# Optimization experiments

Hardware: AMD Instinct MI355X
Metric: run time of the kernel (lower is better)

Reference implementation:

```python
import jax, jax.numpy as jnp
import numpy as np

EMBED_DIM = 128
NUM_HEADS = 4
HEAD_DIM = EMBED_DIM // NUM_HEADS


def setup_inputs() -> dict:
    key = jax.random.key(0)
    ks = jax.random.split(key, 12)
    B, N, D = 4, 4096, EMBED_DIM
    s = 1.0 / np.sqrt(D)
    inp = {
        "query": jax.random.normal(ks[0], (B, N, D), dtype=jnp.float32),
        "key": jax.random.normal(ks[1], (B, N, D), dtype=jnp.float32),
        "value": jax.random.normal(ks[2], (B, N, D), dtype=jnp.float32),
        "Wq": jax.random.uniform(ks[3], (D, D), jnp.float32, -s, s),
        "bq": jax.random.uniform(ks[4], (D,), jnp.float32, -s, s),
        "Wk": jax.random.uniform(ks[5], (D, D), jnp.float32, -s, s),
        "bk": jax.random.uniform(ks[6], (D,), jnp.float32, -s, s),
        "Wv": jax.random.uniform(ks[7], (D, D), jnp.float32, -s, s),
        "bv": jax.random.uniform(ks[8], (D,), jnp.float32, -s, s),
        "Wo": jax.random.uniform(ks[9], (D, D), jnp.float32, -s, s),
        "bo": jax.random.uniform(ks[10], (D,), jnp.float32, -s, s),
    }
    return inp


def reference(query, key, value, Wq, bq, Wk, bk, Wv, bv, Wo, bo):
    B, N, D = query.shape
    H, Dh = NUM_HEADS, HEAD_DIM
    scale = Dh ** -0.5
    # Linear projections (torch Linear: x @ W.T + b), split heads -> [B, H, N, Dh]
    Q = (query @ Wq.T + bq).reshape(B, N, H, Dh).transpose(0, 2, 1, 3)
    K = (key @ Wk.T + bk).reshape(B, N, H, Dh).transpose(0, 2, 1, 3)
    V = (value @ Wv.T + bv).reshape(B, N, H, Dh).transpose(0, 2, 1, 3)
    # Attention scores [B, H, N, N]
    scores = jnp.einsum('bhqd,bhkd->bhqk', Q, K) * scale
    attn = jax.nn.softmax(scores, axis=-1)
    ctx = jnp.einsum('bhqk,bhkd->bhqd', attn, V)  # [B, H, N, Dh]
    ctx = ctx.transpose(0, 2, 1, 3).reshape(B, N, D)
    return ctx @ Wo.T + bo
```

## Files before the change

kernel.cpp:

```cpp
#include <hip/hip_runtime.h>
#include <hip/hip_bf16.h>

#define N_SEQ 4096
#define DIM   128
#define NH    4
#define DH    32
#define BATCH 4

#define QSCALE 0.25503495870989204f

typedef __bf16 bf16x8 __attribute__((ext_vector_type(8)));
typedef __bf16 bf16x2 __attribute__((ext_vector_type(2)));
typedef __bf16 bf16x4 __attribute__((ext_vector_type(4)));
typedef float  f32x4  __attribute__((ext_vector_type(4)));

#define MFMA(a, b, c) __builtin_amdgcn_mfma_f32_16x16x32_bf16((a), (b), (c), 0, 0, 0)

static __device__ __forceinline__ bf16x8 cvt8(const float* __restrict__ p) {
    const float4* f4 = reinterpret_cast<const float4*>(p);
    float4 a = f4[0], b = f4[1];
    bf16x8 r;
    r[0] = (__bf16)a.x; r[1] = (__bf16)a.y; r[2] = (__bf16)a.z; r[3] = (__bf16)a.w;
    r[4] = (__bf16)b.x; r[5] = (__bf16)b.y; r[6] = (__bf16)b.z; r[7] = (__bf16)b.w;
    return r;
}

static __device__ __forceinline__ f32x4 exp4(f32x4 s) {
    f32x4 r;
    r[0] = __builtin_amdgcn_exp2f(s[0]);
    r[1] = __builtin_amdgcn_exp2f(s[1]);
    r[2] = __builtin_amdgcn_exp2f(s[2]);
    r[3] = __builtin_amdgcn_exp2f(s[3]);
    return r;
}

static __device__ __forceinline__ bf16x8 pack8(f32x4 a, f32x4 b) {
    bf16x8 o;
    o[0] = (__bf16)a[0]; o[1] = (__bf16)a[1];
    o[2] = (__bf16)a[2]; o[3] = (__bf16)a[3];
    o[4] = (__bf16)b[0]; o[5] = (__bf16)b[1];
    o[6] = (__bf16)b[2]; o[7] = (__bf16)b[3];
    return o;
}

__global__ __launch_bounds__(256) void proj_qkv(
    const float* __restrict__ xq, const float* __restrict__ xk, const float* __restrict__ xv,
    const float* __restrict__ Wq, const float* __restrict__ Wk, const float* __restrict__ Wv,
    const float* __restrict__ bq, const float* __restrict__ bk, const float* __restrict__ bv,
    __bf16* __restrict__ Qs, __bf16* __restrict__ Kb, __bf16* __restrict__ Vt)
{
    __shared__ __align__(16) char wlds[34816];
    const int z = blockIdx.z;
    const float* x    = (z == 0) ? xq : ((z == 1) ? xk : xv);
    const float* Wf   = (z == 0) ? Wq : ((z == 1) ? Wk : Wv);
    const float* bias = (z == 0) ? bq : ((z == 1) ? bk : bv);
    const int b    = blockIdx.y;
    const int tid  = threadIdx.x;
    const int wave = tid >> 6, lane = tid & 63;
    const int quad = lane >> 4, l15 = lane & 15;
    const int n0   = blockIdx.x * 64 + wave * 16;

    {
        const int r = tid >> 1, half = tid & 1;
        const float* wsrc = Wf + r * DIM + half * 64;
        char* wdst = wlds + r * 272 + half * 128;
        #pragma unroll
        for (int i = 0; i < 8; i++)
            *(bf16x8*)(wdst + i * 16) = cvt8(wsrc + i * 8);
    }

    bf16x8 a[4];
    const float* xrow = x + (b * N_SEQ + n0 + l15) * DIM + quad * 8;
    a[0] = cvt8(xrow);      a[1] = cvt8(xrow + 32);
    a[2] = cvt8(xrow + 64); a[3] = cvt8(xrow + 96);
    __syncthreads();

    const int n = n0 + l15;
    for (int t = 0; t < 8; t++) {
        const char* wr = wlds + (t * 16 + l15) * 272 + quad * 16;
        bf16x8 w0 = *(const bf16x8*)(wr);
        bf16x8 w1 = *(const bf16x8*)(wr + 64);
        bf16x8 w2 = *(const bf16x8*)(wr + 128);
        bf16x8 w3 = *(const bf16x8*)(wr + 192);

        f32x4 acc = {0.f, 0.f, 0.f, 0.f};
        acc = MFMA(w0, a[0], acc);
        acc = MFMA(w1, a[1], acc);
        acc = MFMA(w2, a[2], acc);
        acc = MFMA(w3, a[3], acc);

        const int d0 = t * 16 + quad * 4;
        if (z == 0) {
            const int h = d0 >> 5, dh0 = d0 & 31;
            bf16x4 q4;
            #pragma unroll
            for (int r = 0; r < 4; r++)
                q4[r] = (__bf16)((acc[r] + bias[d0 + r]) * QSCALE);
            *(bf16x4*)(Qs + ((b * NH + h) * N_SEQ + n) * DH + dh0) = q4;
        } else if (z == 1) {
            const int h = d0 >> 5, dh0 = d0 & 31;
            bf16x4 k4;
            #pragma unroll
            for (int r = 0; r < 4; r++)
                k4[r] = (__bf16)(acc[r] + bias[d0 + r]);
            *(bf16x4*)(Kb + ((b * NH + h) * N_SEQ + n) * DH + dh0) = k4;
        } else {
            const int nl = n & 63;
            const int np = (n & ~63) | (nl & 35) | ((nl & 12) << 1) | ((nl & 16) >> 2);
            #pragma unroll
            for (int r = 0; r < 4; r++) {
                const int d = d0 + r, h = d >> 5, dh = d & 31;
                Vt[((b * NH + h) * DH + dh) * N_SEQ + np] = (__bf16)(acc[r] + bias[d]);
            }
        }
    }
}

__global__ __launch_bounds__(256, 2) void flash_attn(
    const __bf16* __restrict__ Qs, const __bf16* __restrict__ Kb,
    const __bf16* __restrict__ Vt, __bf16* __restrict__ ctxb)
{
    __shared__ __align__(16) char smem[77824];
    char* const Kbase = smem;
    char* const Vbase = smem + 40960;

    const int bid  = blockIdx.x;
    const int bh   = bid & 15;
    const int qc   = bid >> 4;
    const int tid  = threadIdx.x;
    const int wave = tid >> 6, lane = tid & 63;
    const int quad = lane >> 4, l15 = lane & 15;
    const int qh   = wave & 1, kh = wave >> 1;
    const int n0   = qc * 128 + qh * 64;
    const int KH   = 2048;

    const __bf16* Qp = Qs + (bh * N_SEQ + n0) * DH;
    bf16x8 qf[4];
    #pragma unroll
    for (int q = 0; q < 4; q++)
        qf[q] = *(const bf16x8*)(Qp + (q * 16 + l15) * DH + quad * 8);

    const int r_ = tid >> 2, c_ = tid & 3;
    const __bf16* gK = Kb + (size_t)bh * N_SEQ * DH + r_ * DH + c_ * 8;
    const __bf16* gV = Vt + ((size_t)bh * DH + (tid >> 3)) * N_SEQ + (tid & 7) * 8;
    const int kofsK = r_ * 80 + c_ * 16;
    const int kofsV = (tid >> 3) * 144 + (tid & 7) * 16;

    {
        #pragma unroll
        for (int g = 0; g < 2; g++) {
            #pragma unroll
            for (int t = 0; t < 2; t++) {
                bf16x8 kr = *(const bf16x8*)(gK + (size_t)(g * KH + t * 64) * DH);
                bf16x8 vr = *(const bf16x8*)(gV + g * KH + t * 64);
                *(bf16x8*)(Kbase + g * 20480 + t * 5120 + kofsK) = kr;
                *(bf16x8*)(Vbase + g * 18432 + t * 4608 + kofsV) = vr;
            }
        }
    }
    __syncthreads();

    char* const Kme = Kbase + kh * 20480;
    char* const Vme = Vbase + kh * 18432;

    f32x4 c[4][2];
    #pragma unroll
    for (int q = 0; q < 4; q++) { c[q][0] = f32x4{0.f,0.f,0.f,0.f}; c[q][1] = f32x4{0.f,0.f,0.f,0.f}; }
    float l[4] = {0.f, 0.f, 0.f, 0.f};
    const f32x4 z4 = {0.f,0.f,0.f,0.f};

    for (int kbb = 0; kbb < KH / 128; kbb++) {
        const int cur = kbb & 1;
        const char* Kc = Kme + cur * 10240;
        const char* Vc = Vme + cur * 9216;

        const int kn = (kbb + 1) & (KH / 128 - 1);
        bf16x8 krn[2][2], vrn[2][2];
        #pragma unroll
        for (int g = 0; g < 2; g++) {
            #pragma unroll
            for (int t = 0; t < 2; t++) {
                krn[g][t] = *(const bf16x8*)(gK + (size_t)(g * KH + kn * 128 + t * 64) * DH);
                vrn[g][t] = *(const bf16x8*)(gV + g * KH + kn * 128 + t * 64);
            }
        }

        #pragma unroll
        for (int t = 0; t < 2; t++) {
            const char* Kt  = Kc + t * 5120;
            const char* Vtl = Vc + t * 4608;

            bf16x8 kf0 = *(const bf16x8*)(Kt + l15 * 80 + quad * 16);
            bf16x8 kf1 = *(const bf16x8*)(Kt + (16 + l15) * 80 + quad * 16);
            bf16x8 kf2 = *(const bf16x8*)(Kt + (32 + l15) * 80 + quad * 16);
            bf16x8 kf3 = *(const bf16x8*)(Kt + (48 + l15) * 80 + quad * 16);

            bf16x8 pf[4][2];
            #pragma unroll
            for (int q = 0; q < 4; q++) {
                f32x4 sa = MFMA(kf0, qf[q], z4);
                f32x4 sb = MFMA(kf1, qf[q], z4);
                f32x4 sc = MFMA(kf2, qf[q], z4);
                f32x4 sd = MFMA(kf3, qf[q], z4);
                f32x4 ea = exp4(sa), eb = exp4(sb), ec = exp4(sc), ed = exp4(sd);
                l[q] += ((ea[0]+ea[1])+(ea[2]+ea[3])) + ((eb[0]+eb[1])+(eb[2]+eb[3]))
                      + ((ec[0]+ec[1])+(ec[2]+ec[3])) + ((ed[0]+ed[1])+(ed[2]+ed[3]));
                pf[q][0] = pack8(ea, eb);
                pf[q][1] = pack8(ec, ed);
            }

            bf16x8 vf00 = *(const bf16x8*)(Vtl + l15 * 144 + quad * 16);
            bf16x8 vf10 = *(const bf16x8*)(Vtl + (16 + l15) * 144 + quad * 16);
            bf16x8 vf01 = *(const bf16x8*)(Vtl + l15 * 144 + 64 + quad * 16);
            bf16x8 vf11 = *(const bf16x8*)(Vtl + (16 + l15) * 144 + 64 + quad * 16);

            #pragma unroll
            for (int q = 0; q < 4; q++) {
                c[q][0] = MFMA(vf00, pf[q][0], c[q][0]);
                c[q][1] = MFMA(vf10, pf[q][0], c[q][1]);
                c[q][0] = MFMA(vf01, pf[q][1], c[q][0]);
                c[q][1] = MFMA(vf11, pf[q][1], c[q][1]);
            }
        }

        #pragma unroll
        for (int g = 0; g < 2; g++) {
            #pragma unroll
            for (int t = 0; t < 2; t++) {
                *(bf16x8*)(Kbase + g * 20480 + (cur ^ 1) * 10240 + t * 5120 + kofsK) = krn[g][t];
                *(bf16x8*)(Vbase + g * 18432 + (cur ^ 1) * 9216 + t * 4608 + kofsV) = vrn[g][t];
            }
        }
        __syncthreads();
    }

    #pragma unroll
    for (int q = 0; q < 4; q++) {
        l[q] += __shfl_xor(l[q], 16);
        l[q] += __shfl_xor(l[q], 32);
    }

    if (kh == 1) {
        char* dst = smem + (qh * 64 + lane) * 144;
        #pragma unroll
        for (int q = 0; q < 4; q++) {
            *(f32x4*)(dst + (q * 2 + 0) * 16) = c[q][0];
            *(f32x4*)(dst + (q * 2 + 1) * 16) = c[q][1];
        }
        f32x4 lv = {l[0], l[1], l[2], l[3]};
        *(f32x4*)(dst + 128) = lv;
    }
    __syncthreads();
    if (kh == 0) {
        const char* src = smem + (qh * 64 + lane) * 144;
        f32x4 lp = *(const f32x4*)(src + 128);
        const int b = bh >> 2, h = bh & 3;
        #pragma unroll
        for (int q = 0; q < 4; q++) {
            c[q][0] += *(const f32x4*)(src + (q * 2 + 0) * 16);
            c[q][1] += *(const f32x4*)(src + (q * 2 + 1) * 16);
            const float inv = 1.0f / (l[q] + lp[q]);
            const int qg = n0 + q * 16 + l15;
            __bf16* dst = ctxb + ((size_t)(b * N_SEQ + qg)) * DIM + h * DH + quad * 4;
            #pragma unroll
            for (int dt = 0; dt < 2; dt++) {
                f32x4 cc = c[q][dt];
                bf16x2 e0 = {(__bf16)(cc[0] * inv), (__bf16)(cc[1] * inv)};
                bf16x2 e1 = {(__bf16)(cc[2] * inv), (__bf16)(cc[3] * inv)};
                *(bf16x2*)(dst + dt * 16)     = e0;
                *(bf16x2*)(dst + dt * 16 + 2) = e1;
            }
        }
    }
}

__global__ __launch_bounds__(256) void out_proj(
    const __bf16* __restrict__ ctxb, const float* __restrict__ Wo,
    const float* __restrict__ bo, float* __restrict__ out)
{
    __shared__ __align__(16) char wlds[34816];
    const int b    = blockIdx.y;
    const int tid  = threadIdx.x;
    const int wave = tid >> 6, lane = tid & 63;
    const int quad = lane >> 4, l15 = lane & 15;
    const int n0   = blockIdx.x * 64 + wave * 16;

    {
        const int r = tid >> 1, half = tid & 1;
        const float* wsrc = Wo + r * DIM + half * 64;
        char* wdst = wlds + r * 272 + half * 128;
        #pragma unroll
        for (int i = 0; i < 8; i++)
            *(bf16x8*)(wdst + i * 16) = cvt8(wsrc + i * 8);
    }

    bf16x8 a[4];
    const __bf16* crow = ctxb + (b * N_SEQ + n0 + l15) * DIM + quad * 8;
    a[0] = *(const bf16x8*)(crow);
    a[1] = *(const bf16x8*)(crow + 32);
    a[2] = *(const bf16x8*)(crow + 64);
    a[3] = *(const bf16x8*)(crow + 96);
    __syncthreads();

    const int n = n0 + l15;
    for (int t = 0; t < 8; t++) {
        const char* wr = wlds + (t * 16 + l15) * 272 + quad * 16;
        bf16x8 w0 = *(const bf16x8*)(wr);
        bf16x8 w1 = *(const bf16x8*)(wr + 64);
        bf16x8 w2 = *(const bf16x8*)(wr + 128);
        bf16x8 w3 = *(const bf16x8*)(wr + 192);

        f32x4 acc = {0.f, 0.f, 0.f, 0.f};
        acc = MFMA(w0, a[0], acc);
        acc = MFMA(w1, a[1], acc);
        acc = MFMA(w2, a[2], acc);
        acc = MFMA(w3, a[3], acc);

        const int d0 = t * 16 + quad * 4;
        float4 o;
        o.x = acc[0] + bo[d0];
        o.y = acc[1] + bo[d0 + 1];
        o.z = acc[2] + bo[d0 + 2];
        o.w = acc[3] + bo[d0 + 3];
        *(float4*)(out + (b * N_SEQ + n) * DIM + d0) = o;
    }
}

extern "C" void kernel_launch(void* const* d_in, const int* in_sizes, int n_in,
                              void* d_out, int out_size, void* d_ws, size_t ws_size,
                              hipStream_t stream)
{
    const float* query = (const float*)d_in[0];
    const float* key   = (const float*)d_in[1];
    const float* value = (const float*)d_in[2];
    const float* Wq = (const float*)d_in[3];
    const float* bq = (const float*)d_in[4];
    const float* Wk = (const float*)d_in[5];
    const float* bk = (const float*)d_in[6];
    const float* Wv = (const float*)d_in[7];
    const float* bv = (const float*)d_in[8];
    const float* Wo = (const float*)d_in[9];
    const float* bo = (const float*)d_in[10];
    float* out = (float*)d_out;

    char* ws = (char*)d_ws;
    const size_t e = (size_t)BATCH * N_SEQ * DIM;
    __bf16* Qs   = (__bf16*)(ws);
    __bf16* Kb   = (__bf16*)(ws + 2 * e);
    __bf16* Vt   = (__bf16*)(ws + 4 * e);
    __bf16* ctxb = (__bf16*)(ws + 6 * e);

    proj_qkv<<<dim3(64, BATCH, 3), 256, 0, stream>>>(
        query, key, value, Wq, Wk, Wv, bq, bk, bv, Qs, Kb, Vt);
    flash_attn<<<dim3(512), 256, 0, stream>>>(Qs, Kb, Vt, ctxb);
    out_proj<<<dim3(64, BATCH), 256, 0, stream>>>(ctxb, Wo, bo, out);
}
```

Measured before the change: 149.7 us.

## Split flash attention keys four ways per block with 64-query blocks

Each block now covers 64 queries instead of 128, and its four waves each take one quarter of the key sequence instead of a 2x2 query/key split. The block count doubles and shared memory drops to about 38KB, so the launch bound is raised to allow four blocks per CU. The double-buffered LDS is replaced by a single buffer: fragments are read into registers, a barrier runs, then the next tile is written, which costs two barriers per step. Row sums are kept as vector accumulators, and the final reduction now merges three partial outputs through LDS instead of one.

```diff
diff --git a/kernel.cpp b/kernel.cpp
--- a/kernel.cpp
+++ b/kernel.cpp
@@ -116,23 +116,22 @@
     }
 }
 
-__global__ __launch_bounds__(256, 2) void flash_attn(
+__global__ __launch_bounds__(256, 4) void flash_attn(
     const __bf16* __restrict__ Qs, const __bf16* __restrict__ Kb,
     const __bf16* __restrict__ Vt, __bf16* __restrict__ ctxb)
 {
-    __shared__ __align__(16) char smem[77824];
+    __shared__ __align__(16) char smem[38912];
     char* const Kbase = smem;
-    char* const Vbase = smem + 40960;
+    char* const Vbase = smem + 20480;
 
     const int bid  = blockIdx.x;
     const int bh   = bid & 15;
     const int qc   = bid >> 4;
     const int tid  = threadIdx.x;
-    const int wave = tid >> 6, lane = tid & 63;
+    const int kh   = tid >> 6, lane = tid & 63;
     const int quad = lane >> 4, l15 = lane & 15;
-    const int qh   = wave & 1, kh = wave >> 1;
-    const int n0   = qc * 128 + qh * 64;
-    const int KH   = 2048;
+    const int n0   = qc * 64;
+    const int KH   = 1024;
 
     const __bf16* Qp = Qs + (bh * N_SEQ + n0) * DH;
     bf16x8 qf[4];
@@ -148,118 +147,111 @@
 
     {
         #pragma unroll
-        for (int g = 0; g < 2; g++) {
-            #pragma unroll
-            for (int t = 0; t < 2; t++) {
-                bf16x8 kr = *(const bf16x8*)(gK + (size_t)(g * KH + t * 64) * DH);
-                bf16x8 vr = *(const bf16x8*)(gV + g * KH + t * 64);
-                *(bf16x8*)(Kbase + g * 20480 + t * 5120 + kofsK) = kr;
-                *(bf16x8*)(Vbase + g * 18432 + t * 4608 + kofsV) = vr;
-            }
+        for (int g = 0; g < 4; g++) {
+            bf16x8 kr = *(const bf16x8*)(gK + (size_t)(g * KH) * DH);
+            bf16x8 vr = *(const bf16x8*)(gV + g * KH);
+            *(bf16x8*)(Kbase + g * 5120 + kofsK) = kr;
+            *(bf16x8*)(Vbase + g * 4608 + kofsV) = vr;
         }
     }
     __syncthreads();
 
-    char* const Kme = Kbase + kh * 20480;
-    char* const Vme = Vbase + kh * 18432;
+    char* const Kme = Kbase + kh * 5120;
+    char* const Vme = Vbase + kh * 4608;
 
     f32x4 c[4][2];
     #pragma unroll
     for (int q = 0; q < 4; q++) { c[q][0] = f32x4{0.f,0.f,0.f,0.f}; c[q][1] = f32x4{0.f,0.f,0.f,0.f}; }
-    float l[4] = {0.f, 0.f, 0.f, 0.f};
+    f32x4 lv[4];
+    #pragma unroll
+    for (int q = 0; q < 4; q++) lv[q] = f32x4{0.f,0.f,0.f,0.f};
     const f32x4 z4 = {0.f,0.f,0.f,0.f};
 
-    for (int kbb = 0; kbb < KH / 128; kbb++) {
-        const int cur = kbb & 1;
-        const char* Kc = Kme + cur * 10240;
-        const char* Vc = Vme + cur * 9216;
-
-        const int kn = (kbb + 1) & (KH / 128 - 1);
-        bf16x8 krn[2][2], vrn[2][2];
-        #pragma unroll
-        for (int g = 0; g < 2; g++) {
-            #pragma unroll
-            for (int t = 0; t < 2; t++) {
-                krn[g][t] = *(const bf16x8*)(gK + (size_t)(g * KH + kn * 128 + t * 64) * DH);
-                vrn[g][t] = *(const bf16x8*)(gV + g * KH + kn * 128 + t * 64);
-            }
-        }
-
-        #pragma unroll
-        for (int t = 0; t < 2; t++) {
-            const char* Kt  = Kc + t * 5120;
-            const char* Vtl = Vc + t * 4608;
-
-            bf16x8 kf0 = *(const bf16x8*)(Kt + l15 * 80 + quad * 16);
-            bf16x8 kf1 = *(const bf16x8*)(Kt + (16 + l15) * 80 + quad * 16);
-            bf16x8 kf2 = *(const bf16x8*)(Kt + (32 + l15) * 80 + quad * 16);
-            bf16x8 kf3 = *(const bf16x8*)(Kt + (48 + l15) * 80 + quad * 16);
-
-            bf16x8 pf[4][2];
-            #pragma unroll
-            for (int q = 0; q < 4; q++) {
-                f32x4 sa = MFMA(kf0, qf[q], z4);
-                f32x4 sb = MFMA(kf1, qf[q], z4);
-                f32x4 sc = MFMA(kf2, qf[q], z4);
-                f32x4 sd = MFMA(kf3, qf[q], z4);
-                f32x4 ea = exp4(sa), eb = exp4(sb), ec = exp4(sc), ed = exp4(sd);
-                l[q] += ((ea[0]+ea[1])+(ea[2]+ea[3])) + ((eb[0]+eb[1])+(eb[2]+eb[3]))
-                      + ((ec[0]+ec[1])+(ec[2]+ec[3])) + ((ed[0]+ed[1])+(ed[2]+ed[3]));
-                pf[q][0] = pack8(ea, eb);
-                pf[q][1] = pack8(ec, ed);
-            }
-
-            bf16x8 vf00 = *(const bf16x8*)(Vtl + l15 * 144 + quad * 16);
-            bf16x8 vf10 = *(const bf16x8*)(Vtl + (16 + l15) * 144 + quad * 16);
-            bf16x8 vf01 = *(const bf16x8*)(Vtl + l15 * 144 + 64 + quad * 16);
-            bf16x8 vf11 = *(const bf16x8*)(Vtl + (16 + l15) * 144 + 64 + quad * 16);
-
-            #pragma unroll
-            for (int q = 0; q < 4; q++) {
-                c[q][0] = MFMA(vf00, pf[q][0], c[q][0]);
-                c[q][1] = MFMA(vf10, pf[q][0], c[q][1]);
-                c[q][0] = MFMA(vf01, pf[q][1], c[q][0]);
-                c[q][1] = MFMA(vf11, pf[q][1], c[q][1]);
-            }
-        }
-
-        #pragma unroll
-        for (int g = 0; g < 2; g++) {
-            #pragma unroll
-            for (int t = 0; t < 2; t++) {
-                *(bf16x8*)(Kbase + g * 20480 + (cur ^ 1) * 10240 + t * 5120 + kofsK) = krn[g][t];
-                *(bf16x8*)(Vbase + g * 18432 + (cur ^ 1) * 9216 + t * 4608 + kofsV) = vrn[g][t];
-            }
-        }
+    for (int kb = 0; kb < KH / 64; kb++) {
+        const int kn = (kb + 1) & (KH / 64 - 1);
+        bf16x8 krn[4], vrn[4];
+        #pragma unroll
+        for (int g = 0; g < 4; g++) {
+            krn[g] = *(const bf16x8*)(gK + (size_t)(g * KH + kn * 64) * DH);
+            vrn[g] = *(const bf16x8*)(gV + g * KH + kn * 64);
+        }
+
+        bf16x8 kf0 = *(const bf16x8*)(Kme + l15 * 80 + quad * 16);
+        bf16x8 kf1 = *(const bf16x8*)(Kme + (16 + l15) * 80 + quad * 16);
+        bf16x8 kf2 = *(const bf16x8*)(Kme + (32 + l15) * 80 + quad * 16);
+        bf16x8 kf3 = *(const bf16x8*)(Kme + (48 + l15) * 80 + quad * 16);
+        bf16x8 vf00 = *(const bf16x8*)(Vme + l15 * 144 + quad * 16);
+        bf16x8 vf10 = *(const bf16x8*)(Vme + (16 + l15) * 144 + quad * 16);
+        bf16x8 vf01 = *(const bf16x8*)(Vme + l15 * 144 + 64 + quad * 16);
+        bf16x8 vf11 = *(const bf16x8*)(Vme + (16 + l15) * 144 + 64 + quad * 16);
+
         __syncthreads();
-    }
-
+
+        #pragma unroll
+        for (int g = 0; g < 4; g++) {
+            *(bf16x8*)(Kbase + g * 5120 + kofsK) = krn[g];
+            *(bf16x8*)(Vbase + g * 4608 + kofsV) = vrn[g];
+        }
+
+        bf16x8 pf[4][2];
+        #pragma unroll
+        for (int q = 0; q < 4; q++) {
+            f32x4 sa = MFMA(kf0, qf[q], z4);
+            f32x4 sb = MFMA(kf1, qf[q], z4);
+            f32x4 sc = MFMA(kf2, qf[q], z4);
+            f32x4 sd = MFMA(kf3, qf[q], z4);
+            f32x4 ea = exp4(sa), eb = exp4(sb), ec = exp4(sc), ed = exp4(sd);
+            lv[q] += (ea + eb) + (ec + ed);
+            pf[q][0] = pack8(ea, eb);
+            pf[q][1] = pack8(ec, ed);
+        }
+
+        #pragma unroll
+        for (int q = 0; q < 4; q++) {
+            c[q][0] = MFMA(vf00, pf[q][0], c[q][0]);
+            c[q][1] = MFMA(vf10, pf[q][0], c[q][1]);
+            c[q][0] = MFMA(vf01, pf[q][1], c[q][0]);
+            c[q][1] = MFMA(vf11, pf[q][1], c[q][1]);
+        }
+
+        __syncthreads();
+    }
+
+    float l[4];
     #pragma unroll
     for (int q = 0; q < 4; q++) {
+        l[q] = (lv[q][0] + lv[q][1]) + (lv[q][2] + lv[q][3]);
         l[q] += __shfl_xor(l[q], 16);
         l[q] += __shfl_xor(l[q], 32);
     }
 
-    if (kh == 1) {
-        char* dst = smem + (qh * 64 + lane) * 144;
+    if (kh != 0) {
+        char* dst = smem + ((kh - 1) * 64 + lane) * 144;
         #pragma unroll
         for (int q = 0; q < 4; q++) {
             *(f32x4*)(dst + (q * 2 + 0) * 16) = c[q][0];
             *(f32x4*)(dst + (q * 2 + 1) * 16) = c[q][1];
         }
-        f32x4 lv = {l[0], l[1], l[2], l[3]};
-        *(f32x4*)(dst + 128) = lv;
+        f32x4 lw = {l[0], l[1], l[2], l[3]};
+        *(f32x4*)(dst + 128) = lw;
     }
     __syncthreads();
     if (kh == 0) {
-        const char* src = smem + (qh * 64 + lane) * 144;
-        f32x4 lp = *(const f32x4*)(src + 128);
+        #pragma unroll
+        for (int m = 0; m < 3; m++) {
+            const char* src = smem + (m * 64 + lane) * 144;
+            #pragma unroll
+            for (int q = 0; q < 4; q++) {
+                c[q][0] += *(const f32x4*)(src + (q * 2 + 0) * 16);
+                c[q][1] += *(const f32x4*)(src + (q * 2 + 1) * 16);
+            }
+            f32x4 lp = *(const f32x4*)(src + 128);
+            l[0] += lp[0]; l[1] += lp[1]; l[2] += lp[2]; l[3] += lp[3];
+        }
         const int b = bh >> 2, h = bh & 3;
         #pragma unroll
         for (int q = 0; q < 4; q++) {
-            c[q][0] += *(const f32x4*)(src + (q * 2 + 0) * 16);
-            c[q][1] += *(const f32x4*)(src + (q * 2 + 1) * 16);
-            const float inv = 1.0f / (l[q] + lp[q]);
+            const float inv = 1.0f / l[q];
             const int qg = n0 + q * 16 + l15;
             __bf16* dst = ctxb + ((size_t)(b * N_SEQ + qg)) * DIM + h * DH + quad * 4;
             #pragma unroll
@@ -352,6 +344,6 @@
 
     proj_qkv<<<dim3(64, BATCH, 3), 256, 0, stream>>>(
         query, key, value, Wq, Wk, Wv, bq, bk, bv, Qs, Kb, Vt);
-    flash_attn<<<dim3(512), 256, 0, stream>>>(Qs, Kb, Vt, ctxb);
+    flash_attn<<<dim3(1024), 256, 0, stream>>>(Qs, Kb, Vt, ctxb);
     out_proj<<<dim3(64, BATCH), 256, 0, stream>>>(ctxb, Wo, bo, out);
 }
```

Measured after the change: 175.5 us. +17.2%, slower.
